# Performance work log

Hardware: AMD Instinct MI355X
Metric: run time of the kernel (lower is better)

Reference implementation:

```python
import jax, jax.numpy as jnp
import numpy as np

B, H, L, D = 16, 8, 512, 64
TEMPERATURE = 8.0  # sqrt(d_k)
MASK_SENTINEL = -10000.0
BIG_NEG = 1e9


def setup_inputs() -> dict:
    key = jax.random.key(0)
    kq, kk, kv, km = jax.random.split(key, 4)
    q = jax.random.normal(kq, (B * H, L, D), dtype=jnp.float32)
    k = jax.random.normal(kk, (B * H, L, D), dtype=jnp.float32)
    v = jax.random.normal(kv, (B * H, L, D), dtype=jnp.float32)
    mask = jnp.where(jax.random.bernoulli(km, 0.1, (B, L)), MASK_SENTINEL, 0.0).astype(jnp.float32)
    return {"q": q, "k": k, "v": v, "mask": mask, "n_head": H}


def reference(q, k, v, mask, n_head):
    # attn: [B*H, L, L]
    attn = jnp.einsum("bid,bjd->bij", q, k) / TEMPERATURE
    # masked_fill(mask == -10000, 1e9); other values subtracted as-is
    m = jnp.where(mask == MASK_SENTINEL, BIG_NEG, mask)          # [B, L]
    m_bh = jnp.repeat(m, n_head, axis=0)                          # [B*H, L], matches reshape(B*H, ...)
    # row mask (mask.unsqueeze(-1).repeat) and its transpose (column mask)
    attn = attn - m_bh[:, :, None] - m_bh[:, None, :]
    attn = jax.nn.softmax(attn, axis=2)
    # dropout in eval mode (identity) for the deterministic reference
    output = jnp.einsum("bij,bjd->bid", attn, v)
    return output, attn
```

## Files before the change

### kernel.cpp

```cpp
#include <hip/hip_runtime.h>
#include <stdint.h>

#define Ln 512
#define Dn 64
#define BHn 128
#define AOFF ((size_t)BHn*Ln*Dn)

typedef __attribute__((ext_vector_type(8))) short short8;
typedef __attribute__((ext_vector_type(4))) float f32x4;
typedef __attribute__((ext_vector_type(4))) unsigned int u32x4;
typedef __attribute__((ext_vector_type(2))) unsigned int u32x2;

#define KSTR  72
#define VTSTR 136
#define PSTRH 136

__device__ __forceinline__ uint16_t f2bf(float f){
  uint32_t x = __float_as_uint(f);
  return (uint16_t)((x + 0x7FFFu + ((x>>16)&1u)) >> 16);
}
__device__ __forceinline__ float bf2f(uint16_t u){ return __uint_as_float(((uint32_t)u)<<16); }
__device__ __forceinline__ uint32_t pack2(float a, float b){
  return (uint32_t)f2bf(a) | ((uint32_t)f2bf(b)<<16);
}

extern "C" __global__ __launch_bounds__(256, 2)
void attn_mfma(const float* __restrict__ qg, const float* __restrict__ kg,
               const float* __restrict__ vg, const float* __restrict__ mg,
               float* __restrict__ outg)
{
  __shared__ uint4 ldsraw[(36864 + 2048)/16];
  uint16_t* KHI = (uint16_t*)ldsraw;
  uint16_t* KLO = KHI + 128*KSTR;
  uint16_t* VT  = (uint16_t*)ldsraw;
  float*    CMV = (float*)((char*)ldsraw + 36864);

  const int t    = threadIdx.x;
  const int lane = t & 63;
  const int wv   = t >> 6;
  const int li   = lane & 15;
  const int lq   = lane >> 4;

  const int lin = blockIdx.x + (blockIdx.y << 3);
  const int xcd = lin & 7;
  const int jj  = lin >> 3;
  const int bh  = (xcd << 4) + (jj >> 3);
  const int b   = bh >> 3;
  const int i0  = (jj & 7)*64 + wv*16;

  const size_t base = (size_t)bh*(Ln*Dn);
  const float* mrow = mg + b*Ln;

  uint16_t* PW = (uint16_t*)((char*)ldsraw + 17408 + wv*(16*PSTRH*2));

  {
    float m0 = mrow[t], m1 = mrow[t+256];
    CMV[t]     = (m0 < -9000.f) ? 1e9f : m0;
    CMV[t+256] = (m1 < -9000.f) ? 1e9f : m1;
  }

  short8 qhi[2], qlo[2];
  {
    const float* qrow = qg + base + (size_t)(i0 + li)*Dn;
    #pragma unroll
    for (int kt=0; kt<2; ++kt){
      const float* p = qrow + kt*32 + lq*8;
      f32x4 x0 = *(const f32x4*)p;
      f32x4 x1 = *(const f32x4*)(p+4);
      #pragma unroll
      for (int e=0; e<8; ++e){
        float x = (e<4) ? x0[e] : x1[e-4];
        uint16_t h = f2bf(x);
        qhi[kt][e] = (short)h;
        qlo[kt][e] = (short)f2bf(x - bf2f(h));
      }
    }
  }

  f32x4 acc[32];
  #pragma unroll
  for (int j=0; j<32; ++j) acc[j] = (f32x4)0.f;

  const int sj = t>>1, skh = t&1;
  #pragma unroll
  for (int c=0; c<4; ++c){
    __syncthreads();
    {
      const float* kr = kg + base + (size_t)(c*128 + sj)*Dn + skh*32;
      uint16_t* dhi = KHI + sj*KSTR + skh*32;
      uint16_t* dlo = KLO + sj*KSTR + skh*32;
      #pragma unroll
      for (int w2=0; w2<4; ++w2){
        f32x4 x0 = *(const f32x4*)(kr + w2*8);
        f32x4 x1 = *(const f32x4*)(kr + w2*8 + 4);
        uint32_t hw[4], lw[4];
        #pragma unroll
        for (int pi=0; pi<4; ++pi){
          float a0 = (pi<2) ? x0[pi*2]   : x1[(pi-2)*2];
          float a1 = (pi<2) ? x0[pi*2+1] : x1[(pi-2)*2+1];
          uint16_t h0 = f2bf(a0), h1 = f2bf(a1);
          hw[pi] = (uint32_t)h0 | ((uint32_t)h1<<16);
          lw[pi] = (uint32_t)f2bf(a0 - bf2f(h0)) | ((uint32_t)f2bf(a1 - bf2f(h1))<<16);
        }
        *(u32x4*)(dhi + w2*8) = (u32x4){hw[0],hw[1],hw[2],hw[3]};
        *(u32x4*)(dlo + w2*8) = (u32x4){lw[0],lw[1],lw[2],lw[3]};
      }
    }
    __syncthreads();
    #pragma unroll
    for (int jt=0; jt<8; ++jt){
      #pragma unroll
      for (int kt=0; kt<2; ++kt){
        const int off = (jt*16 + li)*KSTR + kt*32 + lq*8;
        short8 kh = *(const short8*)(KHI + off);
        short8 kl = *(const short8*)(KLO + off);
        f32x4 A = acc[c*8+jt];
        A = __builtin_amdgcn_mfma_f32_16x16x32_bf16(kh, qhi[kt], A, 0,0,0);
        A = __builtin_amdgcn_mfma_f32_16x16x32_bf16(kl, qhi[kt], A, 0,0,0);
        A = __builtin_amdgcn_mfma_f32_16x16x32_bf16(kh, qlo[kt], A, 0,0,0);
        acc[c*8+jt] = A;
      }
    }
  }

  {
    float mv = mrow[i0 + li];
    const float rmv = (mv < -9000.f) ? 1e9f : mv;
    #pragma unroll
    for (int jt=0; jt<32; ++jt){
      f32x4 cm = *(const f32x4*)(CMV + jt*16 + lq*4);
      #pragma unroll
      for (int r=0; r<4; ++r)
        acc[jt][r] = (acc[jt][r]*0.125f - rmv) - cm[r];
    }
  }
  float mx = -3.4e38f;
  #pragma unroll
  for (int jt=0; jt<32; ++jt)
    #pragma unroll
    for (int r=0; r<4; ++r) mx = fmaxf(mx, acc[jt][r]);
  mx = fmaxf(mx, __shfl_xor(mx, 16));
  mx = fmaxf(mx, __shfl_xor(mx, 32));
  float sum = 0.f;
  #pragma unroll
  for (int jt=0; jt<32; ++jt)
    #pragma unroll
    for (int r=0; r<4; ++r){ float e = __expf(acc[jt][r]-mx); acc[jt][r] = e; sum += e; }
  sum += __shfl_xor(sum, 16);
  sum += __shfl_xor(sum, 32);
  const float inv = 1.0f/sum;

  {
    float* arow = outg + AOFF + (size_t)bh*Ln*Ln + (size_t)(i0+li)*Ln;
    #pragma unroll
    for (int jt=0; jt<32; ++jt){
      f32x4 p = acc[jt]*inv;
      acc[jt] = p;
      *(f32x4*)(arow + jt*16 + lq*4) = p;
    }
  }

  f32x4 oacc[4];
  #pragma unroll
  for (int dt=0; dt<4; ++dt) oacc[dt] = (f32x4)0.f;

  #pragma unroll
  for (int c=0; c<4; ++c){
    __syncthreads();
    #pragma unroll
    for (int it=0; it<2; ++it){
      const int j0 = (t>>4)*4 + it*64;
      const int d0 = (t&15)*4;
      const float* vr = vg + base + (size_t)(c*128 + j0)*Dn + d0;
      f32x4 r0 = *(const f32x4*)(vr);
      f32x4 r1 = *(const f32x4*)(vr + Dn);
      f32x4 r2 = *(const f32x4*)(vr + 2*Dn);
      f32x4 r3 = *(const f32x4*)(vr + 3*Dn);
      #pragma unroll
      for (int qd=0; qd<4; ++qd){
        u32x2 w; w.x = pack2(r0[qd], r1[qd]); w.y = pack2(r2[qd], r3[qd]);
        *(u32x2*)(VT + (d0+qd)*VTSTR + j0) = w;
      }
    }
    __syncthreads();
    #pragma unroll
    for (int jtl=0; jtl<8; ++jtl){
      const f32x4 p = acc[c*8+jtl];
      u32x2 w; w.x = pack2(p[0], p[1]); w.y = pack2(p[2], p[3]);
      *(u32x2*)(PW + li*PSTRH + jtl*16 + lq*4) = w;
    }
    asm volatile("s_waitcnt lgkmcnt(0)" ::: "memory");
    #pragma unroll
    for (int c32=0; c32<4; ++c32){
      short8 pf = *(const short8*)(PW + li*PSTRH + c32*32 + lq*8);
      #pragma unroll
      for (int dt=0; dt<4; ++dt){
        short8 vb = *(const short8*)(VT + (dt*16+li)*VTSTR + c32*32 + lq*8);
        oacc[dt] = __builtin_amdgcn_mfma_f32_16x16x32_bf16(vb, pf, oacc[dt], 0,0,0);
      }
    }
  }

  #pragma unroll
  for (int dt=0; dt<4; ++dt)
    *(f32x4*)(outg + base + (size_t)(i0+li)*Dn + dt*16 + lq*4) = oacc[dt];
}

extern "C" void kernel_launch(void* const* d_in, const int* in_sizes, int n_in,
                              void* d_out, int out_size, void* d_ws, size_t ws_size,
                              hipStream_t stream)
{
  (void)in_sizes; (void)n_in; (void)d_ws; (void)ws_size; (void)out_size;
  dim3 grid(Ln/64, BHn);
  attn_mfma<<<grid, 256, 0, stream>>>((const float*)d_in[0], (const float*)d_in[1],
                                      (const float*)d_in[2], (const float*)d_in[3],
                                      (float*)d_out);
}
```

Before: 241.3 us.

## Split K/V bf16 preconversion into prep kernel and split keys across waves

Adds a prep kernel that converts K into hi/lo bf16 halves and V into transposed bf16 in workspace once per head, instead of every block redoing the conversion in LDS. The main kernel now gives each block 16 query rows and gives each wave a 128-key slice. Softmax max/sum and the PV partial outputs are reduced across waves through LDS. The attention matrix is written with nontemporal stores, and the old single-kernel path is kept as a fallback when the workspace is too small. The cost is an extra launch, workspace traffic and cross-wave reductions, in exchange for a smaller per-block footprint and higher occupancy.

```diff
diff --git a/kernel.cpp b/kernel.cpp
--- a/kernel.cpp
+++ b/kernel.cpp
@@ -11,10 +11,6 @@
 typedef __attribute__((ext_vector_type(4))) unsigned int u32x4;
 typedef __attribute__((ext_vector_type(2))) unsigned int u32x2;
 
-#define KSTR  72
-#define VTSTR 136
-#define PSTRH 136
-
 __device__ __forceinline__ uint16_t f2bf(float f){
   uint32_t x = __float_as_uint(f);
   return (uint16_t)((x + 0x7FFFu + ((x>>16)&1u)) >> 16);
@@ -23,6 +19,216 @@
 __device__ __forceinline__ uint32_t pack2(float a, float b){
   return (uint32_t)f2bf(a) | ((uint32_t)f2bf(b)<<16);
 }
+
+extern "C" __global__ __launch_bounds__(256)
+void attn_prep(const float* __restrict__ kg, const float* __restrict__ vg,
+               uint16_t* __restrict__ khi, uint16_t* __restrict__ klo,
+               uint16_t* __restrict__ vt)
+{
+  const int t  = threadIdx.x;
+  const int c  = blockIdx.x;
+  const int bh = blockIdx.y;
+  const size_t base = (size_t)bh*(Ln*Dn);
+
+  {
+    const int sj  = t>>1, skh = t&1;
+    const float* kr = kg + base + (size_t)(c*128 + sj)*Dn + skh*32;
+    uint16_t* dhi = khi + (size_t)bh*(Ln*Dn) + (size_t)(c*128 + sj)*Dn + skh*32;
+    uint16_t* dlo = klo + (size_t)bh*(Ln*Dn) + (size_t)(c*128 + sj)*Dn + skh*32;
+    #pragma unroll
+    for (int w2=0; w2<4; ++w2){
+      f32x4 x0 = *(const f32x4*)(kr + w2*8);
+      f32x4 x1 = *(const f32x4*)(kr + w2*8 + 4);
+      uint32_t hw[4], lw[4];
+      #pragma unroll
+      for (int pi=0; pi<4; ++pi){
+        float a0 = (pi<2) ? x0[pi*2]   : x1[(pi-2)*2];
+        float a1 = (pi<2) ? x0[pi*2+1] : x1[(pi-2)*2+1];
+        uint16_t h0 = f2bf(a0), h1 = f2bf(a1);
+        hw[pi] = (uint32_t)h0 | ((uint32_t)h1<<16);
+        lw[pi] = (uint32_t)f2bf(a0 - bf2f(h0)) | ((uint32_t)f2bf(a1 - bf2f(h1))<<16);
+      }
+      *(u32x4*)(dhi + w2*8) = (u32x4){hw[0],hw[1],hw[2],hw[3]};
+      *(u32x4*)(dlo + w2*8) = (u32x4){lw[0],lw[1],lw[2],lw[3]};
+    }
+  }
+
+  #pragma unroll
+  for (int it=0; it<2; ++it){
+    const int j0 = (t>>4)*4 + it*64;
+    const int d0 = (t&15)*4;
+    const float* vr = vg + base + (size_t)(c*128 + j0)*Dn + d0;
+    f32x4 r0 = *(const f32x4*)(vr);
+    f32x4 r1 = *(const f32x4*)(vr + Dn);
+    f32x4 r2 = *(const f32x4*)(vr + 2*Dn);
+    f32x4 r3 = *(const f32x4*)(vr + 3*Dn);
+    #pragma unroll
+    for (int qd=0; qd<4; ++qd){
+      u32x2 w; w.x = pack2(r0[qd], r1[qd]); w.y = pack2(r2[qd], r3[qd]);
+      *(u32x2*)(vt + (size_t)bh*(Dn*Ln) + (size_t)(d0+qd)*Ln + c*128 + j0) = w;
+    }
+  }
+}
+
+#define PSTRH 152
+
+extern "C" __global__ __launch_bounds__(256, 4)
+void attn_main(const float* __restrict__ qg, const float* __restrict__ mg,
+               const uint16_t* __restrict__ khi, const uint16_t* __restrict__ klo,
+               const uint16_t* __restrict__ vt, float* __restrict__ outg)
+{
+  __shared__ uint4 lds2[37376/16];
+  uint16_t* PW  = (uint16_t*)lds2;
+  float*    OR_ = (float*)((char*)lds2 + 19456);
+  float*    MXW = (float*)((char*)lds2 + 19456 + 17408);
+  float*    SMW = MXW + 64;
+
+  const int t    = threadIdx.x;
+  const int lane = t & 63;
+  const int wv   = t >> 6;
+  const int li   = lane & 15;
+  const int lq   = lane >> 4;
+
+  const int lin   = blockIdx.x + (blockIdx.y << 5);
+  const int xcd   = lin & 7;
+  const int jj    = lin >> 3;
+  const int bh    = (xcd << 4) + (jj >> 5);
+  const int itile = jj & 31;
+  const int b     = bh >> 3;
+  const int i0    = itile*16;
+  const int wj0   = wv*128;
+
+  const size_t base = (size_t)bh*(Ln*Dn);
+  const float* mrow = mg + b*Ln;
+  uint16_t* PWme = PW + wv*(16*PSTRH);
+
+  short8 qhi[2], qlo[2];
+  {
+    const float* qrow = qg + base + (size_t)(i0 + li)*Dn;
+    #pragma unroll
+    for (int kt=0; kt<2; ++kt){
+      const float* p = qrow + kt*32 + lq*8;
+      f32x4 x0 = *(const f32x4*)p;
+      f32x4 x1 = *(const f32x4*)(p+4);
+      #pragma unroll
+      for (int e=0; e<8; ++e){
+        float x = (e<4) ? x0[e] : x1[e-4];
+        uint16_t h = f2bf(x);
+        qhi[kt][e] = (short)h;
+        qlo[kt][e] = (short)f2bf(x - bf2f(h));
+      }
+    }
+  }
+
+  f32x4 acc[8];
+  #pragma unroll
+  for (int j=0; j<8; ++j) acc[j] = (f32x4)0.f;
+
+  const uint16_t* khb = khi + (size_t)bh*(Ln*Dn) + (size_t)wj0*Dn;
+  const uint16_t* klb = klo + (size_t)bh*(Ln*Dn) + (size_t)wj0*Dn;
+  #pragma unroll
+  for (int jt=0; jt<8; ++jt){
+    const int ro = (jt*16 + li)*Dn;
+    #pragma unroll
+    for (int kt=0; kt<2; ++kt){
+      short8 kh = *(const short8*)(khb + ro + kt*32 + lq*8);
+      short8 kl = *(const short8*)(klb + ro + kt*32 + lq*8);
+      f32x4 A = acc[jt];
+      A = __builtin_amdgcn_mfma_f32_16x16x32_bf16(kh, qhi[kt], A, 0,0,0);
+      A = __builtin_amdgcn_mfma_f32_16x16x32_bf16(kl, qhi[kt], A, 0,0,0);
+      A = __builtin_amdgcn_mfma_f32_16x16x32_bf16(kh, qlo[kt], A, 0,0,0);
+      acc[jt] = A;
+    }
+  }
+
+  {
+    float mv = mrow[i0 + li];
+    const float rmv = (mv < -9000.f) ? 1e9f : mv;
+    #pragma unroll
+    for (int jt=0; jt<8; ++jt){
+      f32x4 cmr = *(const f32x4*)(mrow + wj0 + jt*16 + lq*4);
+      #pragma unroll
+      for (int r=0; r<4; ++r){
+        float cm = (cmr[r] < -9000.f) ? 1e9f : cmr[r];
+        acc[jt][r] = (acc[jt][r]*0.125f - rmv) - cm;
+      }
+    }
+  }
+
+  float mx = -3.4e38f;
+  #pragma unroll
+  for (int jt=0; jt<8; ++jt)
+    #pragma unroll
+    for (int r=0; r<4; ++r) mx = fmaxf(mx, acc[jt][r]);
+  mx = fmaxf(mx, __shfl_xor(mx, 16));
+  mx = fmaxf(mx, __shfl_xor(mx, 32));
+  if (lane < 16) MXW[wv*16 + lane] = mx;
+  __syncthreads();
+  const float mxa = fmaxf(fmaxf(MXW[li], MXW[16+li]), fmaxf(MXW[32+li], MXW[48+li]));
+
+  float sum = 0.f;
+  #pragma unroll
+  for (int jt=0; jt<8; ++jt)
+    #pragma unroll
+    for (int r=0; r<4; ++r){ float e = __expf(acc[jt][r]-mxa); acc[jt][r] = e; sum += e; }
+  sum += __shfl_xor(sum, 16);
+  sum += __shfl_xor(sum, 32);
+  if (lane < 16) SMW[wv*16 + lane] = sum;
+  __syncthreads();
+  const float inv = 1.0f/((SMW[li] + SMW[16+li]) + (SMW[32+li] + SMW[48+li]));
+
+  {
+    float* arow = outg + AOFF + (size_t)bh*Ln*Ln + (size_t)(i0+li)*Ln + wj0;
+    #pragma unroll
+    for (int jt=0; jt<8; ++jt){
+      f32x4 p = acc[jt]*inv;
+      acc[jt] = p;
+      __builtin_nontemporal_store(p, (f32x4*)(arow + jt*16 + lq*4));
+    }
+  }
+
+  #pragma unroll
+  for (int jtl=0; jtl<8; ++jtl){
+    const f32x4 p = acc[jtl];
+    u32x2 w; w.x = pack2(p[0], p[1]); w.y = pack2(p[2], p[3]);
+    *(u32x2*)(PWme + li*PSTRH + jtl*16 + lq*4) = w;
+  }
+  asm volatile("s_waitcnt lgkmcnt(0)" ::: "memory");
+
+  f32x4 oacc[4];
+  #pragma unroll
+  for (int dt=0; dt<4; ++dt) oacc[dt] = (f32x4)0.f;
+
+  const uint16_t* vtb = vt + (size_t)bh*(Dn*Ln) + wj0;
+  #pragma unroll
+  for (int c32=0; c32<4; ++c32){
+    short8 pf = *(const short8*)(PWme + li*PSTRH + c32*32 + lq*8);
+    #pragma unroll
+    for (int dt=0; dt<4; ++dt){
+      short8 vb = *(const short8*)(vtb + (size_t)(dt*16+li)*Ln + c32*32 + lq*8);
+      oacc[dt] = __builtin_amdgcn_mfma_f32_16x16x32_bf16(vb, pf, oacc[dt], 0,0,0);
+    }
+  }
+
+  #pragma unroll
+  for (int dt=0; dt<4; ++dt)
+    #pragma unroll
+    for (int r=0; r<4; ++r)
+      OR_[wv*1088 + (dt*16 + lq*4 + r)*17 + li] = oacc[dt][r];
+  __syncthreads();
+  #pragma unroll
+  for (int k=0; k<4; ++k){
+    const int o = t + 256*k;
+    const int d = o >> 4, i = o & 15;
+    const int x = d*17 + i;
+    float s = (OR_[x] + OR_[1088 + x]) + (OR_[2176 + x] + OR_[3264 + x]);
+    outg[base + (size_t)(i0 + i)*Dn + d] = s;
+  }
+}
+
+#define KSTR  72
+#define VTSTR 136
+#define FPSTRH 136
 
 extern "C" __global__ __launch_bounds__(256, 2)
 void attn_mfma(const float* __restrict__ qg, const float* __restrict__ kg,
@@ -51,7 +257,7 @@
   const size_t base = (size_t)bh*(Ln*Dn);
   const float* mrow = mg + b*Ln;
 
-  uint16_t* PW = (uint16_t*)((char*)ldsraw + 17408 + wv*(16*PSTRH*2));
+  uint16_t* PW = (uint16_t*)((char*)ldsraw + 17408 + wv*(16*FPSTRH*2));
 
   {
     float m0 = mrow[t], m1 = mrow[t+256];
@@ -187,12 +393,12 @@
     for (int jtl=0; jtl<8; ++jtl){
       const f32x4 p = acc[c*8+jtl];
       u32x2 w; w.x = pack2(p[0], p[1]); w.y = pack2(p[2], p[3]);
-      *(u32x2*)(PW + li*PSTRH + jtl*16 + lq*4) = w;
+      *(u32x2*)(PW + li*FPSTRH + jtl*16 + lq*4) = w;
     }
     asm volatile("s_waitcnt lgkmcnt(0)" ::: "memory");
     #pragma unroll
     for (int c32=0; c32<4; ++c32){
-      short8 pf = *(const short8*)(PW + li*PSTRH + c32*32 + lq*8);
+      short8 pf = *(const short8*)(PW + li*FPSTRH + c32*32 + lq*8);
       #pragma unroll
       for (int dt=0; dt<4; ++dt){
         short8 vb = *(const short8*)(VT + (dt*16+li)*VTSTR + c32*32 + lq*8);
@@ -210,9 +416,21 @@
                               void* d_out, int out_size, void* d_ws, size_t ws_size,
                               hipStream_t stream)
 {
-  (void)in_sizes; (void)n_in; (void)d_ws; (void)ws_size; (void)out_size;
-  dim3 grid(Ln/64, BHn);
-  attn_mfma<<<grid, 256, 0, stream>>>((const float*)d_in[0], (const float*)d_in[1],
-                                      (const float*)d_in[2], (const float*)d_in[3],
-                                      (float*)d_out);
-}
+  (void)in_sizes; (void)n_in; (void)out_size;
+  const float* qg = (const float*)d_in[0];
+  const float* kg = (const float*)d_in[1];
+  const float* vg = (const float*)d_in[2];
+  const float* mg = (const float*)d_in[3];
+  float* outg = (float*)d_out;
+
+  const size_t WS_NEED = 25165824;
+  if (d_ws && ws_size >= WS_NEED){
+    uint16_t* khi = (uint16_t*)d_ws;
+    uint16_t* klo = (uint16_t*)((char*)d_ws + 8388608);
+    uint16_t* vt  = (uint16_t*)((char*)d_ws + 16777216);
+    attn_prep<<<dim3(4, BHn), 256, 0, stream>>>(kg, vg, khi, klo, vt);
+    attn_main<<<dim3(32, BHn), 256, 0, stream>>>(qg, mg, khi, klo, vt, outg);
+  } else {
+    attn_mfma<<<dim3(Ln/64, BHn), 256, 0, stream>>>(qg, kg, vg, mg, outg);
+  }
+}
```

New measurement: 294.4 us. 1.22x slower.
